# Kernel tuning notes

Hardware: AMD Instinct MI355X
Metric: run time of the kernel (lower is better)

Reference implementation:

```python
import jax, jax.numpy as jnp
import numpy as np
from jax import lax

T, H = 4096, 2048          # tokens, hidden_size
E, K = 64, 8               # n_routed_experts, top_k
I = 512                    # moe_intermediate_size
IS = 512                   # shared intermediate = moe_intermediate_size * n_shared_experts
ROUTED_SCALING = 2.5


def setup_inputs() -> dict:
    key = jax.random.key(0)
    ks = jax.random.split(key, 6)
    return {
        "hidden_states": jax.random.normal(ks[0], (T, H), jnp.float32),
        "gate_w": jax.random.normal(ks[1], (H, E), jnp.float32) * 0.05,
        "w13": jax.random.normal(ks[2], (E, H, 2 * I), jnp.float32) * 0.02,
        "w2": jax.random.normal(ks[3], (E, I, H), jnp.float32) * 0.02,
        "shared_w13": jax.random.normal(ks[4], (H, 2 * IS), jnp.float32) * 0.02,
        "shared_w2": jax.random.normal(ks[5], (IS, H), jnp.float32) * 0.02,
    }


def reference(hidden_states, gate_w, w13, w2, shared_w13, shared_w2):
    # --- router: sigmoid scoring, grouped top-k with 1 group == plain top-k ---
    logits = hidden_states @ gate_w                        # [T, E]
    scores = jax.nn.sigmoid(logits.astype(jnp.float32))
    topk_w, topk_ids = lax.top_k(scores, K)                # [T, K]
    topk_w = topk_w / jnp.sum(topk_w, axis=-1, keepdims=True)  # renormalize

    # --- dispatch: sort token-expert pairs by expert id, grouped GEMM ---
    flat_ids = topk_ids.reshape(-1)                        # [T*K]
    order = jnp.argsort(flat_ids)                          # pairs grouped by expert
    token_idx = order // K                                 # source token of each sorted pair
    x_sorted = hidden_states[token_idx]                    # [T*K, H]
    group_sizes = jnp.bincount(flat_ids, length=E).astype(jnp.int32)

    gu = lax.ragged_dot(x_sorted, w13, group_sizes)        # [T*K, 2I]
    h = jax.nn.silu(gu[:, :I]) * gu[:, I:]                 # SiluAndMul
    out_sorted = lax.ragged_dot(h, w2, group_sizes)        # [T*K, H]

    # --- combine: unsort, weight, sum over top-k ---
    inv = jnp.argsort(order)
    out_pairs = out_sorted[inv].reshape(T, K, H)
    routed = jnp.sum(out_pairs * topk_w[..., None].astype(out_pairs.dtype), axis=1)

    # --- shared expert MLP ---
    sg = hidden_states @ shared_w13                        # [T, 2*IS]
    shared = (jax.nn.silu(sg[:, :IS]) * sg[:, IS:]) @ shared_w2

    return routed * ROUTED_SCALING + shared
```

## Files before the change

kernel.cpp:

```cpp
#include <hip/hip_runtime.h>
#include <hip/hip_bf16.h>

#define T_TOK 4096
#define HD    2048
#define NE    64
#define TOPK  8
#define IMID  512
#define N13   1024
#define NPAIR (T_TOK*TOPK)
#define NROWS (NPAIR + T_TOK)
#define MAXT1 352
#define RSCALE 2.5f

typedef __attribute__((ext_vector_type(8)))  __bf16 bf16x8;
typedef __attribute__((ext_vector_type(4)))  float  f32x4;

__global__ void init_small(int* __restrict__ counts, int* __restrict__ curs) {
  int tid = threadIdx.x;
  if (tid < NE + 1) { counts[tid] = 0; curs[tid] = 0; }
}
__global__ __launch_bounds__(256) void zero_out_kernel(float4* __restrict__ out4) {
  out4[blockIdx.x * 256 + threadIdx.x] = float4{0.f, 0.f, 0.f, 0.f};
}

__global__ __launch_bounds__(256) void cvt_kernel(const float4* __restrict__ hs4,
                                                  bf16x8* __restrict__ hb8) {
  int gid = blockIdx.x * 256 + threadIdx.x;
  float4 a = hs4[2 * gid], b = hs4[2 * gid + 1];
  bf16x8 v = { (__bf16)a.x, (__bf16)a.y, (__bf16)a.z, (__bf16)a.w,
               (__bf16)b.x, (__bf16)b.y, (__bf16)b.z, (__bf16)b.w };
  hb8[gid] = v;
}

__global__ __launch_bounds__(256) void logits_kernel(const float* __restrict__ hs,
                                                     const float* __restrict__ gw,
                                                     float* __restrict__ logits) {
  __shared__ float hsm[64][16];
  __shared__ float gwm[64][64];
  int tid = threadIdx.x;
  int tb = blockIdx.x * 16;
  int tok = tid >> 4, e4 = (tid & 15) * 4;
  float acc[4] = {0.f, 0.f, 0.f, 0.f};
  for (int c = 0; c < 32; ++c) {
    int kb = c * 64;
    {
      int t16 = tid & 15, kq = tid >> 4;
      float4 f = *(const float4*)&hs[(size_t)(tb + t16) * HD + kb + kq * 4];
      hsm[kq * 4 + 0][t16] = f.x; hsm[kq * 4 + 1][t16] = f.y;
      hsm[kq * 4 + 2][t16] = f.z; hsm[kq * 4 + 3][t16] = f.w;
#pragma unroll
      for (int it = 0; it < 4; ++it) {
        int q = tid + it * 256;
        int gr = q >> 4, gc = (q & 15) * 4;
        *(float4*)&gwm[gr][gc] = *(const float4*)&gw[(size_t)(kb + gr) * NE + gc];
      }
    }
    __syncthreads();
#pragma unroll 8
    for (int k = 0; k < 64; ++k) {
      float h = hsm[k][tok];
      float4 g = *(const float4*)&gwm[k][e4];
      acc[0] += h * g.x; acc[1] += h * g.y; acc[2] += h * g.z; acc[3] += h * g.w;
    }
    __syncthreads();
  }
#pragma unroll
  for (int j = 0; j < 4; ++j) logits[(size_t)(tb + tok) * NE + e4 + j] = acc[j];
}

__global__ __launch_bounds__(256) void top8_kernel(const float* __restrict__ logits,
                                                   int* __restrict__ topk_id,
                                                   float* __restrict__ pair_w,
                                                   int* __restrict__ counts) {
  int lane = threadIdx.x & 63;
  int t = blockIdx.x * 4 + (threadIdx.x >> 6);
  float v = logits[(size_t)t * NE + lane];
  float s = 1.f / (1.f + __expf(-v));
  float cur = s, ssum = 0.f;
  int myid = 0; float myw = 0.f;
  for (int k = 0; k < TOPK; ++k) {
    float bv = cur; int bi = lane;
#pragma unroll
    for (int off = 32; off >= 1; off >>= 1) {
      float ov = __shfl_xor(bv, off);
      int   oi = __shfl_xor(bi, off);
      if (ov > bv || (ov == bv && oi < bi)) { bv = ov; bi = oi; }
    }
    ssum += bv;
    if (lane == k) { myid = bi; myw = bv; }
    if (lane == bi) cur = -1.f;
  }
  if (lane < TOPK) {
    topk_id[(size_t)t * TOPK + lane] = myid;
    pair_w[(size_t)t * TOPK + lane] = myw / ssum * RSCALE;
    atomicAdd(&counts[myid], 1);
  }
}

__global__ void scan_kernel(const int* __restrict__ counts, int* __restrict__ offs,
                            int2* __restrict__ tiles) {
  __shared__ int cnt[65], pref[66], tp[66];
  int tid = threadIdx.x;
  if (tid < 64) cnt[tid] = counts[tid];
  if (tid == 64) cnt[64] = T_TOK;
  __syncthreads();
  if (tid == 0) {
    int o = 0, t = 0;
    for (int e = 0; e <= 64; ++e) {
      pref[e] = o; tp[e] = t;
      o += cnt[e]; t += (cnt[e] + 127) >> 7;
    }
    pref[65] = o; tp[65] = t;
  }
  __syncthreads();
  if (tid <= 64) {
    offs[tid] = pref[tid];
    int c = cnt[tid], base = pref[tid], tb = tp[tid];
    int nt = (c + 127) >> 7;
    for (int i = 0; i < nt; ++i) {
      int rr = c - i * 128; if (rr > 128) rr = 128;
      tiles[tb + i] = make_int2(base + i * 128, (tid << 16) | rr);
    }
  }
  __syncthreads();
  for (int i = tp[65] + tid; i < MAXT1; i += 128) tiles[i] = make_int2(0, 0);
}

__global__ __launch_bounds__(256) void scatter_kernel(const int* __restrict__ topk_id,
                                                      const float* __restrict__ pair_w,
                                                      const int* __restrict__ offs,
                                                      int* __restrict__ curs,
                                                      int* __restrict__ row_token,
                                                      float* __restrict__ row_w,
                                                      int* __restrict__ inv8) {
  int p = blockIdx.x * 256 + threadIdx.x;
  int dst, t; float w;
  if (p < NPAIR) {
    t = p >> 3; int e = topk_id[p]; w = pair_w[p];
    dst = offs[e] + atomicAdd(&curs[e], 1);
    inv8[p] = dst;
  } else {
    t = p - NPAIR; w = 1.0f;
    dst = NPAIR + t;
  }
  row_token[dst] = t;
  row_w[dst] = w;
}

__device__ __forceinline__ int swz(int row, int kbyte) {
  return row * 128 + (kbyte ^ ((row & 7) << 4));
}
__device__ __forceinline__ void glds16(const void* g, void* l) {
  __builtin_amdgcn_global_load_lds((const __attribute__((address_space(1))) void*)g,
                                   (__attribute__((address_space(3))) void*)l, 16, 0, 0);
}
__device__ __forceinline__ void store_bx8(__bf16* Bs, int col, int kbyte, const float* p) {
  bf16x8 v = { (__bf16)p[0], (__bf16)p[1], (__bf16)p[2], (__bf16)p[3],
               (__bf16)p[4], (__bf16)p[5], (__bf16)p[6], (__bf16)p[7] };
  *(bf16x8*)&Bs[swz(col, kbyte) >> 1] = v;
}

#define G1STEP(S, Acur, Anx2, BGc, BUc, BGn, BUn, RL, RS)                                  \
  {                                                                                        \
    if ((S) + 2 < 32) {                                                                    \
      const float* Bn_ = Bp0 + (size_t)((S) + 2) * 64 * N13;                               \
      _Pragma("unroll") for (int r = 0; r < 16; ++r) RL[r] = Bn_[(size_t)r * N13];         \
      __builtin_amdgcn_sched_barrier(0);                                                   \
      _Pragma("unroll") for (int i = 0; i < 2; ++i)                                        \
        glds16(Abase[i] + ((S) + 2) * 64, (Anx2) + wv * 1024 + i * 512);                   \
    }                                                                                      \
    __builtin_amdgcn_sched_barrier(0);                                                     \
    __builtin_amdgcn_s_setprio(1);                                                         \
    _Pragma("unroll") for (int kk = 0; kk < 2; ++kk) {                                     \
      int koff = kk * 64 + lq * 16;                                                        \
      bf16x8 a[2], bg[2], bu[2];                                                           \
      _Pragma("unroll") for (int i = 0; i < 2; ++i)                                        \
        a[i] = *(const bf16x8*)&(Acur)[swz(wrow * 32 + i * 16 + l15, koff) >> 1];          \
      _Pragma("unroll") for (int j = 0; j < 2; ++j) {                                      \
        bg[j] = *(const bf16x8*)&(BGc)[swz(wc * 32 + j * 16 + l15, koff) >> 1];            \
        bu[j] = *(const bf16x8*)&(BUc)[swz(wc * 32 + j * 16 + l15, koff) >> 1];            \
      }                                                                                    \
      _Pragma("unroll") for (int i = 0; i < 2; ++i)                                        \
        _Pragma("unroll") for (int j = 0; j < 2; ++j) {                                    \
          accg[i][j] = __builtin_amdgcn_mfma_f32_16x16x32_bf16(a[i], bg[j], accg[i][j], 0, 0, 0); \
          accu[i][j] = __builtin_amdgcn_mfma_f32_16x16x32_bf16(a[i], bu[j], accu[i][j], 0, 0, 0); \
        }                                                                                  \
    }                                                                                      \
    __builtin_amdgcn_s_setprio(0);                                                         \
    if ((S) + 1 < 32) {                                                                    \
      __bf16* Bmy_ = bm ? (BUn) : (BGn);                                                   \
      store_bx8(Bmy_, bcol, bkq * 32, RS);                                                 \
      store_bx8(Bmy_, bcol, bkq * 32 + 16, RS + 8);                                        \
    }                                                                                      \
    if ((S) + 2 < 32) asm volatile("s_waitcnt vmcnt(18) lgkmcnt(0)" ::: "memory");         \
    else              asm volatile("s_waitcnt vmcnt(0) lgkmcnt(0)"  ::: "memory");         \
    __builtin_amdgcn_s_barrier();                                                          \
    __builtin_amdgcn_sched_barrier(0);                                                     \
  }

__global__ __launch_bounds__(512, 4) void gemm1_kernel(const __bf16* __restrict__ hidden_bf,
                                                       const float* __restrict__ w13,
                                                       const float* __restrict__ sw13,
                                                       const int* __restrict__ row_token,
                                                       const int2* __restrict__ tiles,
                                                       __bf16* __restrict__ hbuf) {
  int2 td = tiles[blockIdx.y];
  int rows = td.y & 0xFFFF;
  if (rows == 0) return;
  int e = td.y >> 16, row0 = td.x;
  const float* W = (e < NE) ? (w13 + (size_t)e * (HD * N13)) : sw13;
  int n0 = blockIdx.x * 64;

  __shared__ __bf16 As0[128 * 64], As1[128 * 64], As2[128 * 64];
  __shared__ __bf16 Bgs[2][64 * 64];
  __shared__ __bf16 Bus[2][64 * 64];

  int tid = threadIdx.x;
  int lane = tid & 63, wv = tid >> 6;
  int wrow = wv >> 1, wc = wv & 1;
  int l15 = lane & 15, lq = lane >> 4;

  int kswz = (((lane & 7) ^ ((lane >> 3) & 7)) << 3);
  const __bf16* Abase[2];
#pragma unroll
  for (int i = 0; i < 2; ++i) {
    int grow = row0 + wv * 16 + i * 8 + (lane >> 3);
    if (grow >= NROWS) grow = NROWS - 1;
    Abase[i] = hidden_bf + (size_t)row_token[grow] * HD + kswz;
  }
  int bm = tid >> 8, bcol = tid & 63, bkq = (tid >> 6) & 3;
  const float* Bp0 = W + (size_t)(bkq * 16) * N13 + (bm ? 512 + n0 : n0) + bcol;

  float pA[16], pB[16];
#pragma unroll
  for (int r = 0; r < 16; ++r) pA[r] = Bp0[(size_t)r * N13];
  __builtin_amdgcn_sched_barrier(0);
#pragma unroll
  for (int i = 0; i < 2; ++i) glds16(Abase[i], As0 + wv * 1024 + i * 512);
  __builtin_amdgcn_sched_barrier(0);
  {
    const float* B1 = Bp0 + (size_t)64 * N13;
#pragma unroll
    for (int r = 0; r < 16; ++r) pB[r] = B1[(size_t)r * N13];
  }
  __builtin_amdgcn_sched_barrier(0);
#pragma unroll
  for (int i = 0; i < 2; ++i) glds16(Abase[i] + 64, As1 + wv * 1024 + i * 512);
  __builtin_amdgcn_sched_barrier(0);
  {
    __bf16* Bmy = bm ? Bus[0] : Bgs[0];
    store_bx8(Bmy, bcol, bkq * 32, pA);
    store_bx8(Bmy, bcol, bkq * 32 + 16, pA + 8);
  }
  asm volatile("s_waitcnt vmcnt(18) lgkmcnt(0)" ::: "memory");
  __builtin_amdgcn_s_barrier();
  __builtin_amdgcn_sched_barrier(0);

  f32x4 accg[2][2], accu[2][2];
#pragma unroll
  for (int i = 0; i < 2; ++i)
#pragma unroll
    for (int j = 0; j < 2; ++j) { accg[i][j] = (f32x4)(0.f); accu[i][j] = (f32x4)(0.f); }

  __bf16 *Ac = As0, *A1 = As1, *A2 = As2;
  for (int s = 0; s < 32; s += 2) {
    G1STEP(s,     Ac, A2, Bgs[0], Bus[0], Bgs[1], Bus[1], pA, pB);
    { __bf16* t = Ac; Ac = A1; A1 = A2; A2 = t; }
    G1STEP(s + 1, Ac, A2, Bgs[1], Bus[1], Bgs[0], Bus[0], pB, pA);
    { __bf16* t = Ac; Ac = A1; A1 = A2; A2 = t; }
  }
#pragma unroll
  for (int mi = 0; mi < 2; ++mi) {
#pragma unroll
    for (int r = 0; r < 4; ++r) {
      int rl = wrow * 32 + mi * 16 + lq * 4 + r;
      if (rl < rows) {
        size_t hrow = (size_t)(row0 + rl) * IMID;
#pragma unroll
        for (int j = 0; j < 2; ++j) {
          float g = accg[mi][j][r], u = accu[mi][j][r];
          float hv = g * u / (1.f + __expf(-g));
          hbuf[hrow + n0 + wc * 32 + j * 16 + l15] = (__bf16)hv;
        }
      }
    }
  }
}

#define G2STEP(S, Acur, Anx2, Bc, Bn, RL, RS)                                              \
  {                                                                                        \
    if ((S) + 2 < 8) {                                                                     \
      const float* Bn_ = Bp0 + (size_t)((S) + 2) * 64 * HD;                                \
      _Pragma("unroll") for (int r = 0; r < 16; ++r) RL[r] = Bn_[(size_t)r * HD];          \
      __builtin_amdgcn_sched_barrier(0);                                                   \
      _Pragma("unroll") for (int i = 0; i < 2; ++i)                                        \
        glds16(Abase[i] + ((S) + 2) * 64, (Anx2) + wv * 1024 + i * 512);                   \
    }                                                                                      \
    __builtin_amdgcn_sched_barrier(0);                                                     \
    __builtin_amdgcn_s_setprio(1);                                                         \
    _Pragma("unroll") for (int kk = 0; kk < 2; ++kk) {                                     \
      int koff = kk * 64 + lq * 16;                                                        \
      bf16x8 a[2], b[4];                                                                   \
      _Pragma("unroll") for (int i = 0; i < 2; ++i)                                        \
        a[i] = *(const bf16x8*)&(Acur)[swz(wrow * 32 + i * 16 + l15, koff) >> 1];          \
      _Pragma("unroll") for (int j = 0; j < 4; ++j)                                        \
        b[j] = *(const bf16x8*)&(Bc)[swz(wc * 64 + j * 16 + l15, koff) >> 1];              \
      _Pragma("unroll") for (int i = 0; i < 2; ++i)                                        \
        _Pragma("unroll") for (int j = 0; j < 4; ++j)                                      \
          acc[i][j] = __builtin_amdgcn_mfma_f32_16x16x32_bf16(a[i], b[j], acc[i][j], 0, 0, 0); \
    }                                                                                      \
    __builtin_amdgcn_s_setprio(0);                                                         \
    if ((S) + 1 < 8) {                                                                     \
      store_bx8((Bn), bcol, bkq * 32, RS);                                                 \
      store_bx8((Bn), bcol, bkq * 32 + 16, RS + 8);                                        \
    }                                                                                      \
    if ((S) + 2 < 8) asm volatile("s_waitcnt vmcnt(18) lgkmcnt(0)" ::: "memory");          \
    else             asm volatile("s_waitcnt vmcnt(0) lgkmcnt(0)"  ::: "memory");          \
    __builtin_amdgcn_s_barrier();                                                          \
    __builtin_amdgcn_sched_barrier(0);                                                     \
  }

template<int MODE>
__global__ __launch_bounds__(512, 4) void gemm2_kernel(const __bf16* __restrict__ hbuf,
                                                       const float* __restrict__ w2,
                                                       const float* __restrict__ sw2,
                                                       const int* __restrict__ row_token,
                                                       const float* __restrict__ row_w,
                                                       const int2* __restrict__ tiles,
                                                       float* __restrict__ dst) {
  int2 td = tiles[blockIdx.y];
  int rows = td.y & 0xFFFF;
  if (rows == 0) return;
  int e = td.y >> 16, row0 = td.x;
  const float* W = (e < NE) ? (w2 + (size_t)e * (IMID * HD)) : sw2;
  int n0 = blockIdx.x * 128;

  __shared__ __bf16 As0[128 * 64], As1[128 * 64], As2[128 * 64];
  __shared__ __bf16 Bs[2][128 * 64];

  int tid = threadIdx.x;
  int lane = tid & 63, wv = tid >> 6;
  int wrow = wv >> 1, wc = wv & 1;
  int l15 = lane & 15, lq = lane >> 4;

  int kswz = (((lane & 7) ^ ((lane >> 3) & 7)) << 3);
  const __bf16* Abase[2];
#pragma unroll
  for (int i = 0; i < 2; ++i) {
    int grow = row0 + wv * 16 + i * 8 + (lane >> 3);
    if (grow >= NROWS) grow = NROWS - 1;
    Abase[i] = hbuf + (size_t)grow * IMID + kswz;
  }
  int bcol = tid & 127, bkq = tid >> 7;
  const float* Bp0 = W + (size_t)(bkq * 16) * HD + n0 + bcol;

  float pA[16], pB[16];
#pragma unroll
  for (int r = 0; r < 16; ++r) pA[r] = Bp0[(size_t)r * HD];
  __builtin_amdgcn_sched_barrier(0);
#pragma unroll
  for (int i = 0; i < 2; ++i) glds16(Abase[i], As0 + wv * 1024 + i * 512);
  __builtin_amdgcn_sched_barrier(0);
  {
    const float* B1 = Bp0 + (size_t)64 * HD;
#pragma unroll
    for (int r = 0; r < 16; ++r) pB[r] = B1[(size_t)r * HD];
  }
  __builtin_amdgcn_sched_barrier(0);
#pragma unroll
  for (int i = 0; i < 2; ++i) glds16(Abase[i] + 64, As1 + wv * 1024 + i * 512);
  __builtin_amdgcn_sched_barrier(0);
  store_bx8(Bs[0], bcol, bkq * 32, pA);
  store_bx8(Bs[0], bcol, bkq * 32 + 16, pA + 8);
  asm volatile("s_waitcnt vmcnt(18) lgkmcnt(0)" ::: "memory");
  __builtin_amdgcn_s_barrier();
  __builtin_amdgcn_sched_barrier(0);

  f32x4 acc[2][4];
#pragma unroll
  for (int i = 0; i < 2; ++i)
#pragma unroll
    for (int j = 0; j < 4; ++j) acc[i][j] = (f32x4)(0.f);

  __bf16 *Ac = As0, *A1 = As1, *A2 = As2;
  for (int s = 0; s < 8; s += 2) {
    G2STEP(s,     Ac, A2, Bs[0], Bs[1], pA, pB);
    { __bf16* t = Ac; Ac = A1; A1 = A2; A2 = t; }
    G2STEP(s + 1, Ac, A2, Bs[1], Bs[0], pB, pA);
    { __bf16* t = Ac; Ac = A1; A1 = A2; A2 = t; }
  }
#pragma unroll
  for (int mi = 0; mi < 2; ++mi) {
#pragma unroll
    for (int r = 0; r < 4; ++r) {
      int rl = wrow * 32 + mi * 16 + lq * 4 + r;
      if (rl < rows) {
        int gr = row0 + rl;
        float wgt = row_w[gr];
        if (MODE == 1) {
          float* prow = dst + (size_t)gr * HD + n0 + wc * 64;
#pragma unroll
          for (int j = 0; j < 4; ++j)
            prow[j * 16 + l15] = acc[mi][j][r] * wgt;
        } else {
          int tok = row_token[gr];
          float* orow = dst + (size_t)tok * HD + n0 + wc * 64;
#pragma unroll
          for (int j = 0; j < 4; ++j)
            atomicAdd(&orow[j * 16 + l15], acc[mi][j][r] * wgt);
        }
      }
    }
  }
}

__global__ __launch_bounds__(256) void combine_kernel(const float* __restrict__ pairout,
                                                      const int* __restrict__ inv8,
                                                      float* __restrict__ out) {
  int t = blockIdx.x;
  int c = threadIdx.x * 8;
  float s0 = 0.f, s1 = 0.f, s2 = 0.f, s3 = 0.f, s4 = 0.f, s5 = 0.f, s6 = 0.f, s7 = 0.f;
#pragma unroll
  for (int k = 0; k < 8; ++k) {
    const float4* pr = (const float4*)(pairout + (size_t)inv8[t * 8 + k] * HD + c);
    float4 a = pr[0], b = pr[1];
    s0 += a.x; s1 += a.y; s2 += a.z; s3 += a.w;
    s4 += b.x; s5 += b.y; s6 += b.z; s7 += b.w;
  }
  {
    const float4* pr = (const float4*)(pairout + (size_t)(NPAIR + t) * HD + c);
    float4 a = pr[0], b = pr[1];
    s0 += a.x; s1 += a.y; s2 += a.z; s3 += a.w;
    s4 += b.x; s5 += b.y; s6 += b.z; s7 += b.w;
  }
  float4* o = (float4*)(out + (size_t)t * HD + c);
  o[0] = float4{s0, s1, s2, s3};
  o[1] = float4{s4, s5, s6, s7};
}

extern "C" void kernel_launch(void* const* d_in, const int* in_sizes, int n_in,
                              void* d_out, int out_size, void* d_ws, size_t ws_size,
                              hipStream_t stream) {
  const float* hidden = (const float*)d_in[0];
  const float* gate_w = (const float*)d_in[1];
  const float* w13    = (const float*)d_in[2];
  const float* w2     = (const float*)d_in[3];
  const float* sw13   = (const float*)d_in[4];
  const float* sw2    = (const float*)d_in[5];
  float* out = (float*)d_out;

  char* ws = (char*)d_ws;
  size_t off = 0;
  __bf16* hbuf      = (__bf16*)(ws + off); off += (size_t)NROWS * IMID * 2;
  __bf16* hidden_bf = (__bf16*)(ws + off); off += (size_t)T_TOK * HD * 2;
  float* logits  = (float*)(ws + off);  off += (size_t)T_TOK * NE * 4;
  int*   topk_id = (int*)(ws + off);    off += (size_t)NPAIR * 4;
  float* pair_w  = (float*)(ws + off);  off += (size_t)NPAIR * 4;
  int*   row_tok = (int*)(ws + off);    off += (size_t)NROWS * 4;
  float* row_w   = (float*)(ws + off);  off += (size_t)NROWS * 4;
  int*   inv8    = (int*)(ws + off);    off += (size_t)NPAIR * 4;
  int*   counts  = (int*)(ws + off);    off += 512;
  int*   curs    = (int*)(ws + off);    off += 512;
  int*   offs    = (int*)(ws + off);    off += 512;
  int2*  tiles   = (int2*)(ws + off);   off += MAXT1 * 8;
  off = (off + 255) & ~(size_t)255;
  float* pairout = (float*)(ws + off);
  size_t need = off + (size_t)NROWS * HD * 4;
  bool rows_path = (ws_size >= need);

  init_small<<<1, 256, 0, stream>>>(counts, curs);
  if (!rows_path)
    zero_out_kernel<<<T_TOK * HD / 4 / 256, 256, 0, stream>>>((float4*)out);
  cvt_kernel<<<T_TOK * HD / 8 / 256, 256, 0, stream>>>((const float4*)hidden, (bf16x8*)hidden_bf);
  logits_kernel<<<T_TOK / 16, 256, 0, stream>>>(hidden, gate_w, logits);
  top8_kernel<<<T_TOK / 4, 256, 0, stream>>>(logits, topk_id, pair_w, counts);
  scan_kernel<<<1, 128, 0, stream>>>(counts, offs, tiles);
  scatter_kernel<<<NROWS / 256, 256, 0, stream>>>(topk_id, pair_w, offs, curs,
                                                  row_tok, row_w, inv8);
  gemm1_kernel<<<dim3(8, MAXT1), 512, 0, stream>>>(hidden_bf, w13, sw13, row_tok, tiles, hbuf);
  if (rows_path) {
    gemm2_kernel<1><<<dim3(16, MAXT1), 512, 0, stream>>>(hbuf, w2, sw2, row_tok, row_w,
                                                         tiles, pairout);
    combine_kernel<<<T_TOK, 256, 0, stream>>>(pairout, inv8, out);
  } else {
    gemm2_kernel<0><<<dim3(16, MAXT1), 512, 0, stream>>>(hbuf, w2, sw2, row_tok, row_w,
                                                         tiles, out);
  }
}
```

Baseline: 773.4 us.

## Halve GEMM workgroup size with 64-row warp tiles, float2 B loads, bf16 pair outputs

Both grouped GEMM kernels now run 256-thread workgroups (4 waves) instead of 512. Each wave computes 64 rows instead of 32, so every B fragment read from LDS feeds more MFMAs. Weight loads become float2 per thread, with two columns converted and stored per thread, and A loads issue four 16-byte LDS copies per wave. Routed pair outputs are written as bf16 rather than fp32, halving the intermediate write/read traffic into the combine kernel at some cost in precision. The trade-offs are higher register pressure from doubled accumulators and lower occupancy from the launch bounds.

Measured after the change: 758.4 us. No clear change (-1.9%).

```diff
diff --git a/kernel.cpp b/kernel.cpp
--- a/kernel.cpp
+++ b/kernel.cpp
@@ -154,33 +154,43 @@
   __builtin_amdgcn_global_load_lds((const __attribute__((address_space(1))) void*)g,
                                    (__attribute__((address_space(3))) void*)l, 16, 0, 0);
 }
-__device__ __forceinline__ void store_bx8(__bf16* Bs, int col, int kbyte, const float* p) {
-  bf16x8 v = { (__bf16)p[0], (__bf16)p[1], (__bf16)p[2], (__bf16)p[3],
-               (__bf16)p[4], (__bf16)p[5], (__bf16)p[6], (__bf16)p[7] };
-  *(bf16x8*)&Bs[swz(col, kbyte) >> 1] = v;
+__device__ __forceinline__ void store_bcols(__bf16* Bs, int c2, int kb, const float2* p) {
+  bf16x8 v0 = { (__bf16)p[0].x, (__bf16)p[1].x, (__bf16)p[2].x, (__bf16)p[3].x,
+                (__bf16)p[4].x, (__bf16)p[5].x, (__bf16)p[6].x, (__bf16)p[7].x };
+  bf16x8 v1 = { (__bf16)p[8].x, (__bf16)p[9].x, (__bf16)p[10].x, (__bf16)p[11].x,
+                (__bf16)p[12].x, (__bf16)p[13].x, (__bf16)p[14].x, (__bf16)p[15].x };
+  bf16x8 w0 = { (__bf16)p[0].y, (__bf16)p[1].y, (__bf16)p[2].y, (__bf16)p[3].y,
+                (__bf16)p[4].y, (__bf16)p[5].y, (__bf16)p[6].y, (__bf16)p[7].y };
+  bf16x8 w1 = { (__bf16)p[8].y, (__bf16)p[9].y, (__bf16)p[10].y, (__bf16)p[11].y,
+                (__bf16)p[12].y, (__bf16)p[13].y, (__bf16)p[14].y, (__bf16)p[15].y };
+  *(bf16x8*)&Bs[swz(c2,     kb)      >> 1] = v0;
+  *(bf16x8*)&Bs[swz(c2,     kb + 16) >> 1] = v1;
+  *(bf16x8*)&Bs[swz(c2 + 1, kb)      >> 1] = w0;
+  *(bf16x8*)&Bs[swz(c2 + 1, kb + 16) >> 1] = w1;
 }
 
 #define G1STEP(S, Acur, Anx2, BGc, BUc, BGn, BUn, RL, RS)                                  \
   {                                                                                        \
     if ((S) + 2 < 32) {                                                                    \
       const float* Bn_ = Bp0 + (size_t)((S) + 2) * 64 * N13;                               \
-      _Pragma("unroll") for (int r = 0; r < 16; ++r) RL[r] = Bn_[(size_t)r * N13];         \
+      _Pragma("unroll") for (int r = 0; r < 16; ++r)                                       \
+        RL[r] = *(const float2*)(Bn_ + (size_t)r * N13);                                   \
       __builtin_amdgcn_sched_barrier(0);                                                   \
-      _Pragma("unroll") for (int i = 0; i < 2; ++i)                                        \
-        glds16(Abase[i] + ((S) + 2) * 64, (Anx2) + wv * 1024 + i * 512);                   \
+      _Pragma("unroll") for (int i = 0; i < 4; ++i)                                        \
+        glds16(Abase[i] + ((S) + 2) * 64, (Anx2) + wv * 2048 + i * 512);                   \
     }                                                                                      \
     __builtin_amdgcn_sched_barrier(0);                                                     \
     __builtin_amdgcn_s_setprio(1);                                                         \
     _Pragma("unroll") for (int kk = 0; kk < 2; ++kk) {                                     \
       int koff = kk * 64 + lq * 16;                                                        \
-      bf16x8 a[2], bg[2], bu[2];                                                           \
-      _Pragma("unroll") for (int i = 0; i < 2; ++i)                                        \
-        a[i] = *(const bf16x8*)&(Acur)[swz(wrow * 32 + i * 16 + l15, koff) >> 1];          \
+      bf16x8 a[4], bg[2], bu[2];                                                           \
+      _Pragma("unroll") for (int i = 0; i < 4; ++i)                                        \
+        a[i] = *(const bf16x8*)&(Acur)[swz(wrow * 64 + i * 16 + l15, koff) >> 1];          \
       _Pragma("unroll") for (int j = 0; j < 2; ++j) {                                      \
         bg[j] = *(const bf16x8*)&(BGc)[swz(wc * 32 + j * 16 + l15, koff) >> 1];            \
         bu[j] = *(const bf16x8*)&(BUc)[swz(wc * 32 + j * 16 + l15, koff) >> 1];            \
       }                                                                                    \
-      _Pragma("unroll") for (int i = 0; i < 2; ++i)                                        \
+      _Pragma("unroll") for (int i = 0; i < 4; ++i)                                        \
         _Pragma("unroll") for (int j = 0; j < 2; ++j) {                                    \
           accg[i][j] = __builtin_amdgcn_mfma_f32_16x16x32_bf16(a[i], bg[j], accg[i][j], 0, 0, 0); \
           accu[i][j] = __builtin_amdgcn_mfma_f32_16x16x32_bf16(a[i], bu[j], accu[i][j], 0, 0, 0); \
@@ -189,16 +199,15 @@
     __builtin_amdgcn_s_setprio(0);                                                         \
     if ((S) + 1 < 32) {                                                                    \
       __bf16* Bmy_ = bm ? (BUn) : (BGn);                                                   \
-      store_bx8(Bmy_, bcol, bkq * 32, RS);                                                 \
-      store_bx8(Bmy_, bcol, bkq * 32 + 16, RS + 8);                                        \
+      store_bcols(Bmy_, c2, kq * 32, RS);                                                  \
     }                                                                                      \
-    if ((S) + 2 < 32) asm volatile("s_waitcnt vmcnt(18) lgkmcnt(0)" ::: "memory");         \
+    if ((S) + 2 < 32) asm volatile("s_waitcnt vmcnt(20) lgkmcnt(0)" ::: "memory");         \
     else              asm volatile("s_waitcnt vmcnt(0) lgkmcnt(0)"  ::: "memory");         \
     __builtin_amdgcn_s_barrier();                                                          \
     __builtin_amdgcn_sched_barrier(0);                                                     \
   }
 
-__global__ __launch_bounds__(512, 4) void gemm1_kernel(const __bf16* __restrict__ hidden_bf,
+__global__ __launch_bounds__(256, 2) void gemm1_kernel(const __bf16* __restrict__ hidden_bf,
                                                        const float* __restrict__ w13,
                                                        const float* __restrict__ sw13,
                                                        const int* __restrict__ row_token,
@@ -221,44 +230,44 @@
   int l15 = lane & 15, lq = lane >> 4;
 
   int kswz = (((lane & 7) ^ ((lane >> 3) & 7)) << 3);
-  const __bf16* Abase[2];
-#pragma unroll
-  for (int i = 0; i < 2; ++i) {
-    int grow = row0 + wv * 16 + i * 8 + (lane >> 3);
+  const __bf16* Abase[4];
+#pragma unroll
+  for (int i = 0; i < 4; ++i) {
+    int grow = row0 + wv * 32 + i * 8 + (lane >> 3);
     if (grow >= NROWS) grow = NROWS - 1;
     Abase[i] = hidden_bf + (size_t)row_token[grow] * HD + kswz;
   }
-  int bm = tid >> 8, bcol = tid & 63, bkq = (tid >> 6) & 3;
-  const float* Bp0 = W + (size_t)(bkq * 16) * N13 + (bm ? 512 + n0 : n0) + bcol;
-
-  float pA[16], pB[16];
-#pragma unroll
-  for (int r = 0; r < 16; ++r) pA[r] = Bp0[(size_t)r * N13];
-  __builtin_amdgcn_sched_barrier(0);
-#pragma unroll
-  for (int i = 0; i < 2; ++i) glds16(Abase[i], As0 + wv * 1024 + i * 512);
+  int bm = tid >> 7, sub = tid & 127;
+  int c2 = (sub & 31) * 2, kq = sub >> 5;
+  const float* Bp0 = W + (size_t)(kq * 16) * N13 + (bm ? 512 + n0 : n0) + c2;
+
+  float2 pA[16], pB[16];
+#pragma unroll
+  for (int r = 0; r < 16; ++r) pA[r] = *(const float2*)(Bp0 + (size_t)r * N13);
+  __builtin_amdgcn_sched_barrier(0);
+#pragma unroll
+  for (int i = 0; i < 4; ++i) glds16(Abase[i], As0 + wv * 2048 + i * 512);
   __builtin_amdgcn_sched_barrier(0);
   {
     const float* B1 = Bp0 + (size_t)64 * N13;
 #pragma unroll
-    for (int r = 0; r < 16; ++r) pB[r] = B1[(size_t)r * N13];
-  }
-  __builtin_amdgcn_sched_barrier(0);
-#pragma unroll
-  for (int i = 0; i < 2; ++i) glds16(Abase[i] + 64, As1 + wv * 1024 + i * 512);
+    for (int r = 0; r < 16; ++r) pB[r] = *(const float2*)(B1 + (size_t)r * N13);
+  }
+  __builtin_amdgcn_sched_barrier(0);
+#pragma unroll
+  for (int i = 0; i < 4; ++i) glds16(Abase[i] + 64, As1 + wv * 2048 + i * 512);
   __builtin_amdgcn_sched_barrier(0);
   {
     __bf16* Bmy = bm ? Bus[0] : Bgs[0];
-    store_bx8(Bmy, bcol, bkq * 32, pA);
-    store_bx8(Bmy, bcol, bkq * 32 + 16, pA + 8);
-  }
-  asm volatile("s_waitcnt vmcnt(18) lgkmcnt(0)" ::: "memory");
+    store_bcols(Bmy, c2, kq * 32, pA);
+  }
+  asm volatile("s_waitcnt vmcnt(20) lgkmcnt(0)" ::: "memory");
   __builtin_amdgcn_s_barrier();
   __builtin_amdgcn_sched_barrier(0);
 
-  f32x4 accg[2][2], accu[2][2];
-#pragma unroll
-  for (int i = 0; i < 2; ++i)
+  f32x4 accg[4][2], accu[4][2];
+#pragma unroll
+  for (int i = 0; i < 4; ++i)
 #pragma unroll
     for (int j = 0; j < 2; ++j) { accg[i][j] = (f32x4)(0.f); accu[i][j] = (f32x4)(0.f); }
 
@@ -270,10 +279,10 @@
     { __bf16* t = Ac; Ac = A1; A1 = A2; A2 = t; }
   }
 #pragma unroll
-  for (int mi = 0; mi < 2; ++mi) {
+  for (int mi = 0; mi < 4; ++mi) {
 #pragma unroll
     for (int r = 0; r < 4; ++r) {
-      int rl = wrow * 32 + mi * 16 + lq * 4 + r;
+      int rl = wrow * 64 + mi * 16 + lq * 4 + r;
       if (rl < rows) {
         size_t hrow = (size_t)(row0 + rl) * IMID;
 #pragma unroll
@@ -291,43 +300,41 @@
   {                                                                                        \
     if ((S) + 2 < 8) {                                                                     \
       const float* Bn_ = Bp0 + (size_t)((S) + 2) * 64 * HD;                                \
-      _Pragma("unroll") for (int r = 0; r < 16; ++r) RL[r] = Bn_[(size_t)r * HD];          \
+      _Pragma("unroll") for (int r = 0; r < 16; ++r)                                       \
+        RL[r] = *(const float2*)(Bn_ + (size_t)r * HD);                                    \
       __builtin_amdgcn_sched_barrier(0);                                                   \
-      _Pragma("unroll") for (int i = 0; i < 2; ++i)                                        \
-        glds16(Abase[i] + ((S) + 2) * 64, (Anx2) + wv * 1024 + i * 512);                   \
+      _Pragma("unroll") for (int i = 0; i < 4; ++i)                                        \
+        glds16(Abase[i] + ((S) + 2) * 64, (Anx2) + wv * 2048 + i * 512);                   \
     }                                                                                      \
     __builtin_amdgcn_sched_barrier(0);                                                     \
     __builtin_amdgcn_s_setprio(1);                                                         \
     _Pragma("unroll") for (int kk = 0; kk < 2; ++kk) {                                     \
       int koff = kk * 64 + lq * 16;                                                        \
-      bf16x8 a[2], b[4];                                                                   \
-      _Pragma("unroll") for (int i = 0; i < 2; ++i)                                        \
-        a[i] = *(const bf16x8*)&(Acur)[swz(wrow * 32 + i * 16 + l15, koff) >> 1];          \
+      bf16x8 a[4], b[4];                                                                   \
+      _Pragma("unroll") for (int i = 0; i < 4; ++i)                                        \
+        a[i] = *(const bf16x8*)&(Acur)[swz(wrow * 64 + i * 16 + l15, koff) >> 1];          \
       _Pragma("unroll") for (int j = 0; j < 4; ++j)                                        \
         b[j] = *(const bf16x8*)&(Bc)[swz(wc * 64 + j * 16 + l15, koff) >> 1];              \
-      _Pragma("unroll") for (int i = 0; i < 2; ++i)                                        \
+      _Pragma("unroll") for (int i = 0; i < 4; ++i)                                        \
         _Pragma("unroll") for (int j = 0; j < 4; ++j)                                      \
           acc[i][j] = __builtin_amdgcn_mfma_f32_16x16x32_bf16(a[i], b[j], acc[i][j], 0, 0, 0); \
     }                                                                                      \
     __builtin_amdgcn_s_setprio(0);                                                         \
-    if ((S) + 1 < 8) {                                                                     \
-      store_bx8((Bn), bcol, bkq * 32, RS);                                                 \
-      store_bx8((Bn), bcol, bkq * 32 + 16, RS + 8);                                        \
-    }                                                                                      \
-    if ((S) + 2 < 8) asm volatile("s_waitcnt vmcnt(18) lgkmcnt(0)" ::: "memory");          \
+    if ((S) + 1 < 8) store_bcols((Bn), c2, kq * 32, RS);                                   \
+    if ((S) + 2 < 8) asm volatile("s_waitcnt vmcnt(20) lgkmcnt(0)" ::: "memory");          \
     else             asm volatile("s_waitcnt vmcnt(0) lgkmcnt(0)"  ::: "memory");          \
     __builtin_amdgcn_s_barrier();                                                          \
     __builtin_amdgcn_sched_barrier(0);                                                     \
   }
 
 template<int MODE>
-__global__ __launch_bounds__(512, 4) void gemm2_kernel(const __bf16* __restrict__ hbuf,
+__global__ __launch_bounds__(256, 2) void gemm2_kernel(const __bf16* __restrict__ hbuf,
                                                        const float* __restrict__ w2,
                                                        const float* __restrict__ sw2,
                                                        const int* __restrict__ row_token,
                                                        const float* __restrict__ row_w,
                                                        const int2* __restrict__ tiles,
-                                                       float* __restrict__ dst) {
+                                                       void* __restrict__ dstv) {
   int2 td = tiles[blockIdx.y];
   int rows = td.y & 0xFFFF;
   if (rows == 0) return;
@@ -344,41 +351,40 @@
   int l15 = lane & 15, lq = lane >> 4;
 
   int kswz = (((lane & 7) ^ ((lane >> 3) & 7)) << 3);
-  const __bf16* Abase[2];
-#pragma unroll
-  for (int i = 0; i < 2; ++i) {
-    int grow = row0 + wv * 16 + i * 8 + (lane >> 3);
+  const __bf16* Abase[4];
+#pragma unroll
+  for (int i = 0; i < 4; ++i) {
+    int grow = row0 + wv * 32 + i * 8 + (lane >> 3);
     if (grow >= NROWS) grow = NROWS - 1;
     Abase[i] = hbuf + (size_t)grow * IMID + kswz;
   }
-  int bcol = tid & 127, bkq = tid >> 7;
-  const float* Bp0 = W + (size_t)(bkq * 16) * HD + n0 + bcol;
-
-  float pA[16], pB[16];
-#pragma unroll
-  for (int r = 0; r < 16; ++r) pA[r] = Bp0[(size_t)r * HD];
-  __builtin_amdgcn_sched_barrier(0);
-#pragma unroll
-  for (int i = 0; i < 2; ++i) glds16(Abase[i], As0 + wv * 1024 + i * 512);
+  int c2 = (tid & 63) * 2, kq = tid >> 6;
+  const float* Bp0 = W + (size_t)(kq * 16) * HD + n0 + c2;
+
+  float2 pA[16], pB[16];
+#pragma unroll
+  for (int r = 0; r < 16; ++r) pA[r] = *(const float2*)(Bp0 + (size_t)r * HD);
+  __builtin_amdgcn_sched_barrier(0);
+#pragma unroll
+  for (int i = 0; i < 4; ++i) glds16(Abase[i], As0 + wv * 2048 + i * 512);
   __builtin_amdgcn_sched_barrier(0);
   {
     const float* B1 = Bp0 + (size_t)64 * HD;
 #pragma unroll
-    for (int r = 0; r < 16; ++r) pB[r] = B1[(size_t)r * HD];
-  }
-  __builtin_amdgcn_sched_barrier(0);
-#pragma unroll
-  for (int i = 0; i < 2; ++i) glds16(Abase[i] + 64, As1 + wv * 1024 + i * 512);
-  __builtin_amdgcn_sched_barrier(0);
-  store_bx8(Bs[0], bcol, bkq * 32, pA);
-  store_bx8(Bs[0], bcol, bkq * 32 + 16, pA + 8);
-  asm volatile("s_waitcnt vmcnt(18) lgkmcnt(0)" ::: "memory");
+    for (int r = 0; r < 16; ++r) pB[r] = *(const float2*)(B1 + (size_t)r * HD);
+  }
+  __builtin_amdgcn_sched_barrier(0);
+#pragma unroll
+  for (int i = 0; i < 4; ++i) glds16(Abase[i] + 64, As1 + wv * 2048 + i * 512);
+  __builtin_amdgcn_sched_barrier(0);
+  store_bcols(Bs[0], c2, kq * 32, pA);
+  asm volatile("s_waitcnt vmcnt(20) lgkmcnt(0)" ::: "memory");
   __builtin_amdgcn_s_barrier();
   __builtin_amdgcn_sched_barrier(0);
 
-  f32x4 acc[2][4];
-#pragma unroll
-  for (int i = 0; i < 2; ++i)
+  f32x4 acc[4][4];
+#pragma unroll
+  for (int i = 0; i < 4; ++i)
 #pragma unroll
     for (int j = 0; j < 4; ++j) acc[i][j] = (f32x4)(0.f);
 
@@ -390,21 +396,21 @@
     { __bf16* t = Ac; Ac = A1; A1 = A2; A2 = t; }
   }
 #pragma unroll
-  for (int mi = 0; mi < 2; ++mi) {
+  for (int mi = 0; mi < 4; ++mi) {
 #pragma unroll
     for (int r = 0; r < 4; ++r) {
-      int rl = wrow * 32 + mi * 16 + lq * 4 + r;
+      int rl = wrow * 64 + mi * 16 + lq * 4 + r;
       if (rl < rows) {
         int gr = row0 + rl;
         float wgt = row_w[gr];
         if (MODE == 1) {
-          float* prow = dst + (size_t)gr * HD + n0 + wc * 64;
+          __bf16* prow = (__bf16*)dstv + (size_t)gr * HD + n0 + wc * 64;
 #pragma unroll
           for (int j = 0; j < 4; ++j)
-            prow[j * 16 + l15] = acc[mi][j][r] * wgt;
+            prow[j * 16 + l15] = (__bf16)(acc[mi][j][r] * wgt);
         } else {
           int tok = row_token[gr];
-          float* orow = dst + (size_t)tok * HD + n0 + wc * 64;
+          float* orow = (float*)dstv + (size_t)tok * HD + n0 + wc * 64;
 #pragma unroll
           for (int j = 0; j < 4; ++j)
             atomicAdd(&orow[j * 16 + l15], acc[mi][j][r] * wgt);
@@ -414,7 +420,7 @@
   }
 }
 
-__global__ __launch_bounds__(256) void combine_kernel(const float* __restrict__ pairout,
+__global__ __launch_bounds__(256) void combine_kernel(const __bf16* __restrict__ pairout,
                                                       const int* __restrict__ inv8,
                                                       float* __restrict__ out) {
   int t = blockIdx.x;
@@ -422,16 +428,14 @@
   float s0 = 0.f, s1 = 0.f, s2 = 0.f, s3 = 0.f, s4 = 0.f, s5 = 0.f, s6 = 0.f, s7 = 0.f;
 #pragma unroll
   for (int k = 0; k < 8; ++k) {
-    const float4* pr = (const float4*)(pairout + (size_t)inv8[t * 8 + k] * HD + c);
-    float4 a = pr[0], b = pr[1];
-    s0 += a.x; s1 += a.y; s2 += a.z; s3 += a.w;
-    s4 += b.x; s5 += b.y; s6 += b.z; s7 += b.w;
+    bf16x8 v = *(const bf16x8*)(pairout + (size_t)inv8[t * 8 + k] * HD + c);
+    s0 += (float)v[0]; s1 += (float)v[1]; s2 += (float)v[2]; s3 += (float)v[3];
+    s4 += (float)v[4]; s5 += (float)v[5]; s6 += (float)v[6]; s7 += (float)v[7];
   }
   {
-    const float4* pr = (const float4*)(pairout + (size_t)(NPAIR + t) * HD + c);
-    float4 a = pr[0], b = pr[1];
-    s0 += a.x; s1 += a.y; s2 += a.z; s3 += a.w;
-    s4 += b.x; s5 += b.y; s6 += b.z; s7 += b.w;
+    bf16x8 v = *(const bf16x8*)(pairout + (size_t)(NPAIR + t) * HD + c);
+    s0 += (float)v[0]; s1 += (float)v[1]; s2 += (float)v[2]; s3 += (float)v[3];
+    s4 += (float)v[4]; s5 += (float)v[5]; s6 += (float)v[6]; s7 += (float)v[7];
   }
   float4* o = (float4*)(out + (size_t)t * HD + c);
   o[0] = float4{s0, s1, s2, s3};
@@ -464,8 +468,8 @@
   int*   offs    = (int*)(ws + off);    off += 512;
   int2*  tiles   = (int2*)(ws + off);   off += MAXT1 * 8;
   off = (off + 255) & ~(size_t)255;
-  float* pairout = (float*)(ws + off);
-  size_t need = off + (size_t)NROWS * HD * 4;
+  __bf16* pairout = (__bf16*)(ws + off);
+  size_t need = off + (size_t)NROWS * HD * 2;
   bool rows_path = (ws_size >= need);
 
   init_small<<<1, 256, 0, stream>>>(counts, curs);
@@ -477,13 +481,13 @@
   scan_kernel<<<1, 128, 0, stream>>>(counts, offs, tiles);
   scatter_kernel<<<NROWS / 256, 256, 0, stream>>>(topk_id, pair_w, offs, curs,
                                                   row_tok, row_w, inv8);
-  gemm1_kernel<<<dim3(8, MAXT1), 512, 0, stream>>>(hidden_bf, w13, sw13, row_tok, tiles, hbuf);
+  gemm1_kernel<<<dim3(8, MAXT1), 256, 0, stream>>>(hidden_bf, w13, sw13, row_tok, tiles, hbuf);
   if (rows_path) {
-    gemm2_kernel<1><<<dim3(16, MAXT1), 512, 0, stream>>>(hbuf, w2, sw2, row_tok, row_w,
-                                                         tiles, pairout);
+    gemm2_kernel<1><<<dim3(16, MAXT1), 256, 0, stream>>>(hbuf, w2, sw2, row_tok, row_w,
+                                                         tiles, (void*)pairout);
     combine_kernel<<<T_TOK, 256, 0, stream>>>(pairout, inv8, out);
   } else {
-    gemm2_kernel<0><<<dim3(16, MAXT1), 512, 0, stream>>>(hbuf, w2, sw2, row_tok, row_w,
-                                                         tiles, out);
-  }
-}
+    gemm2_kernel<0><<<dim3(16, MAXT1), 256, 0, stream>>>(hbuf, w2, sw2, row_tok, row_w,
+                                                         tiles, (void*)out);
+  }
+}
```

## Pre-convert expert weights to bf16 and store pair outputs in bf16

Applied to the files above, without the earlier changes.

Adds per-call conversion kernels that turn w13, w2 and the shared weights from fp32 into bf16 in workspace, and templates both grouped GEMMs on the weight type so they load bf16 weights. The intermediate per-pair output buffer and the combine kernel also switch to bf16, and launch bounds drop from 4 to 2 blocks per SU. The goal is to halve weight and pair-output traffic inside the GEMMs and combine. In exchange, every call must read all fp32 weights (about 805 MB) and write them back as bf16, which may cost more than it saves. The bf16 pair outputs also lose precision.

Result: slower. 872.4 us (+12.8%).

```diff
diff --git a/kernel.cpp b/kernel.cpp
--- a/kernel.cpp
+++ b/kernel.cpp
@@ -15,6 +15,7 @@
 typedef __attribute__((ext_vector_type(8)))  __bf16 bf16x8;
 typedef __attribute__((ext_vector_type(4)))  float  f32x4;
 
+
 __global__ void init_small(int* __restrict__ counts, int* __restrict__ curs) {
   int tid = threadIdx.x;
   if (tid < NE + 1) { counts[tid] = 0; curs[tid] = 0; }
@@ -23,13 +24,13 @@
   out4[blockIdx.x * 256 + threadIdx.x] = float4{0.f, 0.f, 0.f, 0.f};
 }
 
-__global__ __launch_bounds__(256) void cvt_kernel(const float4* __restrict__ hs4,
-                                                  bf16x8* __restrict__ hb8) {
+__global__ __launch_bounds__(256) void cvt_kernel(const float4* __restrict__ src4,
+                                                  bf16x8* __restrict__ dst8) {
   int gid = blockIdx.x * 256 + threadIdx.x;
-  float4 a = hs4[2 * gid], b = hs4[2 * gid + 1];
+  float4 a = src4[2 * gid], b = src4[2 * gid + 1];
   bf16x8 v = { (__bf16)a.x, (__bf16)a.y, (__bf16)a.z, (__bf16)a.w,
                (__bf16)b.x, (__bf16)b.y, (__bf16)b.z, (__bf16)b.w };
-  hb8[gid] = v;
+  dst8[gid] = v;
 }
 
 __global__ __launch_bounds__(256) void logits_kernel(const float* __restrict__ hs,
@@ -159,11 +160,15 @@
                (__bf16)p[4], (__bf16)p[5], (__bf16)p[6], (__bf16)p[7] };
   *(bf16x8*)&Bs[swz(col, kbyte) >> 1] = v;
 }
+__device__ __forceinline__ void store_bx8(__bf16* Bs, int col, int kbyte, const __bf16* p) {
+  bf16x8 v = { p[0], p[1], p[2], p[3], p[4], p[5], p[6], p[7] };
+  *(bf16x8*)&Bs[swz(col, kbyte) >> 1] = v;
+}
 
 #define G1STEP(S, Acur, Anx2, BGc, BUc, BGn, BUn, RL, RS)                                  \
   {                                                                                        \
     if ((S) + 2 < 32) {                                                                    \
-      const float* Bn_ = Bp0 + (size_t)((S) + 2) * 64 * N13;                               \
+      const TB* Bn_ = Bp0 + (size_t)((S) + 2) * 64 * N13;                                  \
       _Pragma("unroll") for (int r = 0; r < 16; ++r) RL[r] = Bn_[(size_t)r * N13];         \
       __builtin_amdgcn_sched_barrier(0);                                                   \
       _Pragma("unroll") for (int i = 0; i < 2; ++i)                                        \
@@ -198,9 +203,10 @@
     __builtin_amdgcn_sched_barrier(0);                                                     \
   }
 
-__global__ __launch_bounds__(512, 4) void gemm1_kernel(const __bf16* __restrict__ hidden_bf,
-                                                       const float* __restrict__ w13,
-                                                       const float* __restrict__ sw13,
+template<typename TB>
+__global__ __launch_bounds__(512, 2) void gemm1_kernel(const __bf16* __restrict__ hidden_bf,
+                                                       const TB* __restrict__ w13,
+                                                       const TB* __restrict__ sw13,
                                                        const int* __restrict__ row_token,
                                                        const int2* __restrict__ tiles,
                                                        __bf16* __restrict__ hbuf) {
@@ -208,7 +214,7 @@
   int rows = td.y & 0xFFFF;
   if (rows == 0) return;
   int e = td.y >> 16, row0 = td.x;
-  const float* W = (e < NE) ? (w13 + (size_t)e * (HD * N13)) : sw13;
+  const TB* W = (e < NE) ? (w13 + (size_t)e * (HD * N13)) : sw13;
   int n0 = blockIdx.x * 64;
 
   __shared__ __bf16 As0[128 * 64], As1[128 * 64], As2[128 * 64];
@@ -229,9 +235,9 @@
     Abase[i] = hidden_bf + (size_t)row_token[grow] * HD + kswz;
   }
   int bm = tid >> 8, bcol = tid & 63, bkq = (tid >> 6) & 3;
-  const float* Bp0 = W + (size_t)(bkq * 16) * N13 + (bm ? 512 + n0 : n0) + bcol;
-
-  float pA[16], pB[16];
+  const TB* Bp0 = W + (size_t)(bkq * 16) * N13 + (bm ? 512 + n0 : n0) + bcol;
+
+  TB pA[16], pB[16];
 #pragma unroll
   for (int r = 0; r < 16; ++r) pA[r] = Bp0[(size_t)r * N13];
   __builtin_amdgcn_sched_barrier(0);
@@ -239,7 +245,7 @@
   for (int i = 0; i < 2; ++i) glds16(Abase[i], As0 + wv * 1024 + i * 512);
   __builtin_amdgcn_sched_barrier(0);
   {
-    const float* B1 = Bp0 + (size_t)64 * N13;
+    const TB* B1 = Bp0 + (size_t)64 * N13;
 #pragma unroll
     for (int r = 0; r < 16; ++r) pB[r] = B1[(size_t)r * N13];
   }
@@ -290,7 +296,7 @@
 #define G2STEP(S, Acur, Anx2, Bc, Bn, RL, RS)                                              \
   {                                                                                        \
     if ((S) + 2 < 8) {                                                                     \
-      const float* Bn_ = Bp0 + (size_t)((S) + 2) * 64 * HD;                                \
+      const TB* Bn_ = Bp0 + (size_t)((S) + 2) * 64 * HD;                                   \
       _Pragma("unroll") for (int r = 0; r < 16; ++r) RL[r] = Bn_[(size_t)r * HD];          \
       __builtin_amdgcn_sched_barrier(0);                                                   \
       _Pragma("unroll") for (int i = 0; i < 2; ++i)                                        \
@@ -320,19 +326,19 @@
     __builtin_amdgcn_sched_barrier(0);                                                     \
   }
 
-template<int MODE>
-__global__ __launch_bounds__(512, 4) void gemm2_kernel(const __bf16* __restrict__ hbuf,
-                                                       const float* __restrict__ w2,
-                                                       const float* __restrict__ sw2,
+template<typename TB, int MODE>
+__global__ __launch_bounds__(512, 2) void gemm2_kernel(const __bf16* __restrict__ hbuf,
+                                                       const TB* __restrict__ w2,
+                                                       const TB* __restrict__ sw2,
                                                        const int* __restrict__ row_token,
                                                        const float* __restrict__ row_w,
                                                        const int2* __restrict__ tiles,
-                                                       float* __restrict__ dst) {
+                                                       void* __restrict__ dstv) {
   int2 td = tiles[blockIdx.y];
   int rows = td.y & 0xFFFF;
   if (rows == 0) return;
   int e = td.y >> 16, row0 = td.x;
-  const float* W = (e < NE) ? (w2 + (size_t)e * (IMID * HD)) : sw2;
+  const TB* W = (e < NE) ? (w2 + (size_t)e * (IMID * HD)) : sw2;
   int n0 = blockIdx.x * 128;
 
   __shared__ __bf16 As0[128 * 64], As1[128 * 64], As2[128 * 64];
@@ -352,9 +358,9 @@
     Abase[i] = hbuf + (size_t)grow * IMID + kswz;
   }
   int bcol = tid & 127, bkq = tid >> 7;
-  const float* Bp0 = W + (size_t)(bkq * 16) * HD + n0 + bcol;
-
-  float pA[16], pB[16];
+  const TB* Bp0 = W + (size_t)(bkq * 16) * HD + n0 + bcol;
+
+  TB pA[16], pB[16];
 #pragma unroll
   for (int r = 0; r < 16; ++r) pA[r] = Bp0[(size_t)r * HD];
   __builtin_amdgcn_sched_barrier(0);
@@ -362,7 +368,7 @@
   for (int i = 0; i < 2; ++i) glds16(Abase[i], As0 + wv * 1024 + i * 512);
   __builtin_amdgcn_sched_barrier(0);
   {
-    const float* B1 = Bp0 + (size_t)64 * HD;
+    const TB* B1 = Bp0 + (size_t)64 * HD;
 #pragma unroll
     for (int r = 0; r < 16; ++r) pB[r] = B1[(size_t)r * HD];
   }
@@ -398,13 +404,13 @@
         int gr = row0 + rl;
         float wgt = row_w[gr];
         if (MODE == 1) {
-          float* prow = dst + (size_t)gr * HD + n0 + wc * 64;
+          __bf16* prow = (__bf16*)dstv + (size_t)gr * HD + n0 + wc * 64;
 #pragma unroll
           for (int j = 0; j < 4; ++j)
-            prow[j * 16 + l15] = acc[mi][j][r] * wgt;
+            prow[j * 16 + l15] = (__bf16)(acc[mi][j][r] * wgt);
         } else {
           int tok = row_token[gr];
-          float* orow = dst + (size_t)tok * HD + n0 + wc * 64;
+          float* orow = (float*)dstv + (size_t)tok * HD + n0 + wc * 64;
 #pragma unroll
           for (int j = 0; j < 4; ++j)
             atomicAdd(&orow[j * 16 + l15], acc[mi][j][r] * wgt);
@@ -414,7 +420,7 @@
   }
 }
 
-__global__ __launch_bounds__(256) void combine_kernel(const float* __restrict__ pairout,
+__global__ __launch_bounds__(256) void combine_kernel(const __bf16* __restrict__ pairout,
                                                       const int* __restrict__ inv8,
                                                       float* __restrict__ out) {
   int t = blockIdx.x;
@@ -422,16 +428,14 @@
   float s0 = 0.f, s1 = 0.f, s2 = 0.f, s3 = 0.f, s4 = 0.f, s5 = 0.f, s6 = 0.f, s7 = 0.f;
 #pragma unroll
   for (int k = 0; k < 8; ++k) {
-    const float4* pr = (const float4*)(pairout + (size_t)inv8[t * 8 + k] * HD + c);
-    float4 a = pr[0], b = pr[1];
-    s0 += a.x; s1 += a.y; s2 += a.z; s3 += a.w;
-    s4 += b.x; s5 += b.y; s6 += b.z; s7 += b.w;
+    bf16x8 v = *(const bf16x8*)(pairout + (size_t)inv8[t * 8 + k] * HD + c);
+    s0 += (float)v[0]; s1 += (float)v[1]; s2 += (float)v[2]; s3 += (float)v[3];
+    s4 += (float)v[4]; s5 += (float)v[5]; s6 += (float)v[6]; s7 += (float)v[7];
   }
   {
-    const float4* pr = (const float4*)(pairout + (size_t)(NPAIR + t) * HD + c);
-    float4 a = pr[0], b = pr[1];
-    s0 += a.x; s1 += a.y; s2 += a.z; s3 += a.w;
-    s4 += b.x; s5 += b.y; s6 += b.z; s7 += b.w;
+    bf16x8 v = *(const bf16x8*)(pairout + (size_t)(NPAIR + t) * HD + c);
+    s0 += (float)v[0]; s1 += (float)v[1]; s2 += (float)v[2]; s3 += (float)v[3];
+    s4 += (float)v[4]; s5 += (float)v[5]; s6 += (float)v[6]; s7 += (float)v[7];
   }
   float4* o = (float4*)(out + (size_t)t * HD + c);
   o[0] = float4{s0, s1, s2, s3};
@@ -464,26 +468,53 @@
   int*   offs    = (int*)(ws + off);    off += 512;
   int2*  tiles   = (int2*)(ws + off);   off += MAXT1 * 8;
   off = (off + 255) & ~(size_t)255;
-  float* pairout = (float*)(ws + off);
-  size_t need = off + (size_t)NROWS * HD * 4;
-  bool rows_path = (ws_size >= need);
+  __bf16* pairout = (__bf16*)(ws + off);
+  size_t need_rows = off + (size_t)NROWS * HD * 2;
+  bool rows_path = (ws_size >= need_rows);
+  size_t woff = (need_rows + 255) & ~(size_t)255;
+  __bf16* w13b  = (__bf16*)(ws + woff);
+  __bf16* w2b   = w13b + (size_t)NE * HD * N13;
+  __bf16* sw13b = w2b + (size_t)NE * IMID * HD;
+  __bf16* sw2b  = sw13b + (size_t)HD * N13;
+  size_t welems = (size_t)NE * HD * N13 + (size_t)NE * IMID * HD
+                + (size_t)HD * N13 + (size_t)IMID * HD;
+  bool wfit = rows_path && (ws_size >= woff + welems * 2);
 
   init_small<<<1, 256, 0, stream>>>(counts, curs);
   if (!rows_path)
     zero_out_kernel<<<T_TOK * HD / 4 / 256, 256, 0, stream>>>((float4*)out);
   cvt_kernel<<<T_TOK * HD / 8 / 256, 256, 0, stream>>>((const float4*)hidden, (bf16x8*)hidden_bf);
+  if (wfit) {
+    cvt_kernel<<<(int)((size_t)NE * HD * N13 / 8 / 256), 256, 0, stream>>>(
+        (const float4*)w13, (bf16x8*)w13b);
+    cvt_kernel<<<(int)((size_t)NE * IMID * HD / 8 / 256), 256, 0, stream>>>(
+        (const float4*)w2, (bf16x8*)w2b);
+    cvt_kernel<<<(int)((size_t)HD * N13 / 8 / 256), 256, 0, stream>>>(
+        (const float4*)sw13, (bf16x8*)sw13b);
+    cvt_kernel<<<(int)((size_t)IMID * HD / 8 / 256), 256, 0, stream>>>(
+        (const float4*)sw2, (bf16x8*)sw2b);
+  }
   logits_kernel<<<T_TOK / 16, 256, 0, stream>>>(hidden, gate_w, logits);
   top8_kernel<<<T_TOK / 4, 256, 0, stream>>>(logits, topk_id, pair_w, counts);
   scan_kernel<<<1, 128, 0, stream>>>(counts, offs, tiles);
   scatter_kernel<<<NROWS / 256, 256, 0, stream>>>(topk_id, pair_w, offs, curs,
                                                   row_tok, row_w, inv8);
-  gemm1_kernel<<<dim3(8, MAXT1), 512, 0, stream>>>(hidden_bf, w13, sw13, row_tok, tiles, hbuf);
-  if (rows_path) {
-    gemm2_kernel<1><<<dim3(16, MAXT1), 512, 0, stream>>>(hbuf, w2, sw2, row_tok, row_w,
-                                                         tiles, pairout);
+  if (wfit) {
+    gemm1_kernel<__bf16><<<dim3(8, MAXT1), 512, 0, stream>>>(hidden_bf, w13b, sw13b,
+                                                             row_tok, tiles, hbuf);
+    gemm2_kernel<__bf16, 1><<<dim3(16, MAXT1), 512, 0, stream>>>(hbuf, w2b, sw2b, row_tok,
+                                                                 row_w, tiles, (void*)pairout);
     combine_kernel<<<T_TOK, 256, 0, stream>>>(pairout, inv8, out);
   } else {
-    gemm2_kernel<0><<<dim3(16, MAXT1), 512, 0, stream>>>(hbuf, w2, sw2, row_tok, row_w,
-                                                         tiles, out);
-  }
-}
+    gemm1_kernel<float><<<dim3(8, MAXT1), 512, 0, stream>>>(hidden_bf, w13, sw13,
+                                                            row_tok, tiles, hbuf);
+    if (rows_path) {
+      gemm2_kernel<float, 1><<<dim3(16, MAXT1), 512, 0, stream>>>(hbuf, w2, sw2, row_tok,
+                                                                  row_w, tiles, (void*)pairout);
+      combine_kernel<<<T_TOK, 256, 0, stream>>>(pairout, inv8, out);
+    } else {
+      gemm2_kernel<float, 0><<<dim3(16, MAXT1), 512, 0, stream>>>(hbuf, w2, sw2, row_tok,
+                                                                  row_w, tiles, (void*)out);
+    }
+  }
+}
```
